# Performance work log

Hardware: AMD Instinct MI355X
Metric: run time of the kernel (lower is better)

The kernel has to match this reference:

```python
import jax, jax.numpy as jnp
import numpy as np

B, C_IN, T, IMG, P = 4, 3, 8, 224, 16
E, DEPTH, D_INNER, N_ST, DT_R, K = 384, 24, 768, 16, 24, 4
HP = IMG // P
NP_ = HP * HP          # 196 patches per frame
L = T * NP_            # 1568 tokens
EPS = 1e-5


def setup_inputs():
    key = jax.random.key(0)
    ks = jax.random.split(key, 24)
    r = lambda k, s, sc=0.02: jax.random.normal(k, s, jnp.float32) * sc
    inp = {
        "x": jax.random.normal(ks[0], (B, C_IN, T, IMG, IMG), jnp.float32),
        "patch_w": r(ks[1], (E, C_IN, 1, P, P)),
        "patch_b": jnp.zeros((E,), jnp.float32),
        "pos_embed": r(ks[2], (NP_, E)),
        "temporal_pos": r(ks[3], (T, E)),
        "imp_w1": r(ks[4], (E, E)),
        "imp_b1": jnp.zeros((E,), jnp.float32),
        "imp_w2": r(ks[5], (1, E)),
        "imp_b2": jnp.zeros((1,), jnp.float32),
        "in_w": r(ks[6], (DEPTH, 2 * D_INNER, E)),
        "out_w": r(ks[7], (DEPTH, E, D_INNER)),
        "norm_w": jnp.ones((DEPTH, E), jnp.float32),
        "norm_f_w": jnp.ones((E,), jnp.float32),
    }
    A_row = jnp.log(jnp.arange(1, N_ST + 1, dtype=jnp.float32))  # S4D-real init
    for i, sfx in enumerate(["", "_b"]):
        b = 8 + 4 * i
        inp["conv_w" + sfx] = r(ks[b], (DEPTH, D_INNER, K), 0.1)
        inp["conv_b" + sfx] = jnp.zeros((DEPTH, D_INNER), jnp.float32)
        inp["xp_w" + sfx] = r(ks[b + 1], (DEPTH, DT_R + 2 * N_ST, D_INNER))
        inp["dt_w" + sfx] = r(ks[b + 2], (DEPTH, D_INNER, DT_R), 0.01)
        inp["dt_b" + sfx] = jax.random.uniform(ks[b + 3], (DEPTH, D_INNER), jnp.float32, -4.6, -2.3)
        inp["A_log" + sfx] = jnp.tile(A_row, (DEPTH, D_INNER, 1))
        inp["D" + sfx] = jnp.ones((DEPTH, D_INNER), jnp.float32)
    return inp


def rmsnorm(x, w):
    x = x.astype(jnp.float32)
    return x * jax.lax.rsqrt(jnp.mean(x * x, axis=-1, keepdims=True) + EPS) * w


def causal_conv1d(x, w, b):
    # x: [B,L,D]; depthwise causal conv with kernel K
    xt = x.transpose(0, 2, 1)  # B D L
    y = jax.lax.conv_general_dilated(
        xt, w[:, None, :], (1,), [(K - 1, 0)],
        dimension_numbers=("NCH", "OIH", "NCH"), feature_group_count=D_INNER)
    return (y + b[None, :, None]).transpose(0, 2, 1)


def selective_scan(xt, dt, Bm, Cm, A, Dp):
    # xt,dt: [B,L,D]; Bm,Cm: [B,L,N]; A: [D,N]
    def step(h, ins):
        dt_t, x_t, B_t, C_t = ins  # [B,D],[B,D],[B,N],[B,N]
        h = h * jnp.exp(dt_t[..., None] * A) + (dt_t * x_t)[..., None] * B_t[:, None, :]
        return h, jnp.einsum('bdn,bn->bd', h, C_t)
    h0 = jnp.zeros((xt.shape[0], D_INNER, N_ST), xt.dtype)
    xs = (dt.transpose(1, 0, 2), xt.transpose(1, 0, 2),
          Bm.transpose(1, 0, 2), Cm.transpose(1, 0, 2))
    _, ys = jax.lax.scan(step, h0, xs)
    return ys.transpose(1, 0, 2) + xt * Dp


def mamba_dir(xc, z, cw, cb, xpw, dtw, dtb, Alog, Dp):
    xt = jax.nn.silu(causal_conv1d(xc, cw, cb))
    dbc = jnp.einsum('bld,ed->ble', xt, xpw)
    dt_low = dbc[..., :DT_R]
    Bm = dbc[..., DT_R:DT_R + N_ST]
    Cm = dbc[..., DT_R + N_ST:]
    dt = jax.nn.softplus(jnp.einsum('blr,dr->bld', dt_low, dtw) + dtb)
    y = selective_scan(xt, dt, Bm, Cm, -jnp.exp(Alog), Dp)
    return y * jax.nn.silu(z)


def mamba_block(h, p):
    xz = jnp.einsum('ble,fe->blf', h, p['in_w'])
    xc, z = xz[..., :D_INNER], xz[..., D_INNER:]
    yf = mamba_dir(xc, z, p['conv_w'], p['conv_b'], p['xp_w'], p['dt_w'], p['dt_b'], p['A_log'], p['D'])
    flip = lambda t: t[:, ::-1, :]
    yb = flip(mamba_dir(flip(xc), flip(z), p['conv_w_b'], p['conv_b_b'], p['xp_w_b'],
                        p['dt_w_b'], p['dt_b_b'], p['A_log_b'], p['D_b']))
    return jnp.einsum('bld,ed->ble', yf + yb, p['out_w'])


def _encoder(x, patch_w, patch_b, pos_embed, temporal_pos, imp_w1, imp_b1, imp_w2, imp_b2,
             in_w, out_w, norm_w, norm_f_w,
             conv_w, conv_b, xp_w, dt_w, dt_b, A_log, D,
             conv_w_b, conv_b_b, xp_w_b, dt_w_b, dt_b_b, A_log_b, D_b, mixer=mamba_block):
    Bn = x.shape[0]
    # PatchEmbed: Conv3d kernel (1,P,P) stride (1,P,P) == patchify + matmul
    xp = x.reshape(Bn, C_IN, T, HP, P, HP, P)
    xp = xp.transpose(0, 2, 3, 5, 1, 4, 6).reshape(Bn, T, NP_, C_IN * P * P)
    tok = xp @ patch_w.reshape(E, C_IN * P * P).T + patch_b  # [B,T,N,E]
    tok = tok + pos_embed[None, None] + temporal_pos[None, :, None, :]
    xseq = tok.reshape(Bn, L, E)
    # token importance gating
    h1 = jax.nn.relu(xseq @ imp_w1.T + imp_b1)
    logits = (h1 @ imp_w2.T + imp_b2)[..., 0]  # [B,L]
    xseq = xseq * jax.nn.sigmoid(logits)[..., None]
    stacked = {'in_w': in_w, 'out_w': out_w, 'norm_w': norm_w,
               'conv_w': conv_w, 'conv_b': conv_b, 'xp_w': xp_w, 'dt_w': dt_w,
               'dt_b': dt_b, 'A_log': A_log, 'D': D,
               'conv_w_b': conv_w_b, 'conv_b_b': conv_b_b, 'xp_w_b': xp_w_b,
               'dt_w_b': dt_w_b, 'dt_b_b': dt_b_b, 'A_log_b': A_log_b, 'D_b': D_b}

    def layer_fn(carry, p):
        hidden, residual = carry
        residual = (hidden + residual).astype(jnp.float32)  # fused add-norm, prenorm
        hn = rmsnorm(residual, p['norm_w'])
        hidden = mixer(hn, p)
        return (hidden, residual), None

    (hidden, residual), _ = jax.lax.scan(layer_fn, (xseq, jnp.zeros_like(xseq)), stacked)
    feats = rmsnorm(hidden + residual, norm_f_w)
    return feats, logits


def reference(x, patch_w, patch_b, pos_embed, temporal_pos, imp_w1, imp_b1, imp_w2, imp_b2,
              in_w, out_w, norm_w, norm_f_w,
              conv_w, conv_b, xp_w, dt_w, dt_b, A_log, D,
              conv_w_b, conv_b_b, xp_w_b, dt_w_b, dt_b_b, A_log_b, D_b):
    return _encoder(x, patch_w, patch_b, pos_embed, temporal_pos, imp_w1, imp_b1, imp_w2, imp_b2,
                    in_w, out_w, norm_w, norm_f_w,
                    conv_w, conv_b, xp_w, dt_w, dt_b, A_log, D,
                    conv_w_b, conv_b_b, xp_w_b, dt_w_b, dt_b_b, A_log_b, D_b)
```

## Files before the change

### kernel.cpp

```cpp
#include <hip/hip_runtime.h>
#include <hip/hip_bf16.h>

#define LL 1568
#define EE 384
#define DD 768
#define BB 4

typedef float f32x4 __attribute__((ext_vector_type(4)));
typedef float f32x2 __attribute__((ext_vector_type(2)));
typedef unsigned short u16x2 __attribute__((ext_vector_type(2)));
typedef unsigned short u16x4 __attribute__((ext_vector_type(4)));
typedef unsigned short u16x8 __attribute__((ext_vector_type(8)));
typedef __bf16 bf16x8 __attribute__((ext_vector_type(8)));

__device__ inline unsigned short f2bf(float f) {
    unsigned int u = __builtin_bit_cast(unsigned int, f);
    u += 0x7fffu + ((u >> 16) & 1u);
    return (unsigned short)(u >> 16);
}
__device__ inline float bf2f(unsigned short u) {
    unsigned int v = ((unsigned int)u) << 16;
    return __builtin_bit_cast(float, v);
}
__device__ inline float silu_f(float v) { return v / (1.f + __expf(-v)); }
__device__ inline float exp2_f(float v) { return __builtin_amdgcn_exp2f(v); }

__global__ __launch_bounds__(256) void k_cvt(const float* __restrict__ src,
                                             unsigned short* __restrict__ dst, int n4) {
    int i = blockIdx.x * 256 + threadIdx.x;
    int stride = gridDim.x * 256;
    for (; i < n4; i += stride) {
        f32x4 v = *(const f32x4*)(src + (size_t)i * 4);
        u16x4 o;
#pragma unroll
        for (int j = 0; j < 4; j++) o[j] = f2bf(v[j]);
        *(u16x4*)(dst + (size_t)i * 4) = o;
    }
}

__global__ __launch_bounds__(256) void k_pad_xpw(const float* __restrict__ src,
                                                 unsigned short* __restrict__ dst) {
    const int total = 24 * 64 * 768;
    for (int i = blockIdx.x * 256 + threadIdx.x; i < total; i += gridDim.x * 256) {
        int l = i / (64 * 768);
        int r = (i / 768) % 64;
        int dcol = i % 768;
        dst[i] = (r < 56) ? f2bf(src[((size_t)l * 56 + r) * 768 + dcol]) : (unsigned short)0;
    }
}

__global__ __launch_bounds__(256) void k_pad_dtw(const float* __restrict__ src,
                                                 unsigned short* __restrict__ dst) {
    const int total = 24 * 768 * 32;
    for (int i = blockIdx.x * 256 + threadIdx.x; i < total; i += gridDim.x * 256) {
        int kk = i & 31;
        int nrow = i >> 5;
        dst[i] = (kk < 24) ? f2bf(src[(size_t)nrow * 24 + kk]) : (unsigned short)0;
    }
}

__global__ __launch_bounds__(256) void k_patch(const float* __restrict__ x,
                                               unsigned short* __restrict__ patches) {
    int bid = blockIdx.x;
    int b = bid / LL, rr = bid % LL, t = rr / 196, pp = rr % 196, hp = pp / 14, wp = pp % 14;
    for (int k = threadIdx.x; k < 768; k += 256) {
        int c = k >> 8, rem = k & 255, i = rem >> 4, j = rem & 15;
        patches[(size_t)bid * 768 + k] =
            f2bf(x[(((size_t)(b * 3 + c) * 8 + t) * 224 + hp * 16 + i) * 224 + wp * 16 + j]);
    }
}

template <int EPI, bool ASUM, bool OUTBF>
__global__ __launch_bounds__(256) void k_gemm(
    const unsigned short* __restrict__ A, const unsigned short* __restrict__ A2,
    const unsigned short* __restrict__ W, const unsigned short* __restrict__ W2,
    float* __restrict__ C, unsigned short* __restrict__ Cb, int K, int ldc,
    const float* __restrict__ bias, const float* __restrict__ bias2,
    const float* __restrict__ pos, const float* __restrict__ tpos) {
    const int tid = threadIdx.x;
    const int m0 = blockIdx.y * 128;
    const int n0 = blockIdx.x * 128;
    __shared__ unsigned short As[128 * 40];
    __shared__ unsigned short Ws[128 * 40];
    const int sr = tid >> 2;
    const int skc = tid & 3;

    const unsigned short* Wp = W;
    const float* biasp = bias;
    if constexpr (EPI == 3) {
        if (m0 >= 6272) { Wp = W2; biasp = bias2; }
    }

    f32x4 acc[4][4];
#pragma unroll
    for (int mi = 0; mi < 4; mi++)
#pragma unroll
        for (int ni = 0; ni < 4; ni++) acc[mi][ni] = (f32x4){0.f, 0.f, 0.f, 0.f};

    const int lane = tid & 63;
    const int wv = tid >> 6;
    const int wm = (wv & 1) << 6;
    const int wn = (wv >> 1) << 6;
    const int lr = lane & 15;
    const int kg = lane >> 4;

    u16x8 ar[2], wr_[2];
    auto loadT = [&](int kt) {
#pragma unroll
        for (int i = 0; i < 2; i++) {
            size_t ka = (size_t)(m0 + sr + 64 * i) * K + kt * 32 + skc * 8;
            u16x8 v = *(const u16x8*)(A + ka);
            if constexpr (ASUM) {
                u16x8 v2 = *(const u16x8*)(A2 + ka);
#pragma unroll
                for (int j = 0; j < 8; j++) v[j] = f2bf(bf2f(v[j]) + bf2f(v2[j]));
            }
            ar[i] = v;
            wr_[i] = *(const u16x8*)(Wp + (size_t)(n0 + sr + 64 * i) * K + kt * 32 + skc * 8);
        }
    };

    const int nK = K >> 5;
    loadT(0);
    for (int kt = 0; kt < nK; ++kt) {
#pragma unroll
        for (int i = 0; i < 2; i++) {
            *(u16x8*)&As[(sr + 64 * i) * 40 + skc * 8] = ar[i];
            *(u16x8*)&Ws[(sr + 64 * i) * 40 + skc * 8] = wr_[i];
        }
        __syncthreads();
        if (kt + 1 < nK) loadT(kt + 1);
        bf16x8 af[4], bfm[4];
#pragma unroll
        for (int mi = 0; mi < 4; mi++)
            af[mi] = *(const bf16x8*)&As[(wm + mi * 16 + lr) * 40 + kg * 8];
#pragma unroll
        for (int ni = 0; ni < 4; ni++)
            bfm[ni] = *(const bf16x8*)&Ws[(wn + ni * 16 + lr) * 40 + kg * 8];
#pragma unroll
        for (int mi = 0; mi < 4; mi++)
#pragma unroll
            for (int ni = 0; ni < 4; ni++)
                acc[mi][ni] = __builtin_amdgcn_mfma_f32_16x16x32_bf16(af[mi], bfm[ni], acc[mi][ni], 0, 0, 0);
        __syncthreads();
    }

#pragma unroll
    for (int mi = 0; mi < 4; mi++)
#pragma unroll
        for (int ni = 0; ni < 4; ni++)
#pragma unroll
            for (int j = 0; j < 4; j++) {
                int m = m0 + wm + mi * 16 + kg * 4 + j;
                int n = n0 + wn + ni * 16 + lr;
                float v = acc[mi][ni][j];
                if constexpr (EPI == 1) {
                    int rr = m % LL;
                    int t = rr / 196, p = rr % 196;
                    v += bias[n] + pos[p * EE + n] + tpos[t * EE + n];
                    C[(size_t)m * ldc + n] = v;
                    Cb[(size_t)m * ldc + n] = f2bf(v);
                } else if constexpr (EPI == 2) {
                    v += bias[n];
                    v = fmaxf(v, 0.f);
                    C[(size_t)m * ldc + n] = v;
                } else if constexpr (EPI == 3) {
                    v += biasp[n];
                    float sp = (v > 20.f) ? v : log1pf(__expf(v));
                    Cb[(size_t)m * ldc + n] = f2bf(sp);
                } else {
                    if constexpr (OUTBF)
                        Cb[(size_t)m * ldc + n] = f2bf(v);
                    else
                        C[(size_t)m * ldc + n] = v;
                }
            }
}

__global__ __launch_bounds__(64) void k_logits(const float* __restrict__ h1, const float* __restrict__ w2,
                                               const float* __restrict__ b2, float* __restrict__ xseq,
                                               float* __restrict__ logits_out) {
    int row = blockIdx.x;
    int lane = threadIdx.x;
    float acc = 0.f;
#pragma unroll
    for (int i = 0; i < 6; i++) {
        int e = lane + i * 64;
        acc += h1[(size_t)row * EE + e] * w2[e];
    }
#pragma unroll
    for (int off = 32; off >= 1; off >>= 1) acc += __shfl_xor(acc, off);
    float logit = acc + b2[0];
    if (lane == 0) logits_out[row] = logit;
    float sg = 1.f / (1.f + __expf(-logit));
#pragma unroll
    for (int i = 0; i < 6; i++) {
        int e = lane + i * 64;
        xseq[(size_t)row * EE + e] *= sg;
    }
}

template <bool OBF>
__global__ __launch_bounds__(256) void k_norm(const float* __restrict__ hidden, float* __restrict__ resid,
                                              const float* __restrict__ wn, float* __restrict__ outf,
                                              unsigned short* __restrict__ outb,
                                              int first, int writeResid) {
    int row = blockIdx.x * 4 + (threadIdx.x >> 6);
    int lane = threadIdx.x & 63;
    size_t base = (size_t)row * EE;
    float v[6];
    float ss = 0.f;
#pragma unroll
    for (int i = 0; i < 6; i++) {
        int e = lane + i * 64;
        float h = hidden[base + e];
        float r = first ? 0.f : resid[base + e];
        float s = h + r;
        v[i] = s;
        ss += s * s;
    }
#pragma unroll
    for (int off = 32; off >= 1; off >>= 1) ss += __shfl_xor(ss, off);
    if (writeResid) {
#pragma unroll
        for (int i = 0; i < 6; i++) resid[base + lane + i * 64] = v[i];
    }
    float sc = rsqrtf(ss * (1.f / 384.f) + 1e-5f);
#pragma unroll
    for (int i = 0; i < 6; i++) {
        int e = lane + i * 64;
        float o = v[i] * sc * wn[e];
        if constexpr (OBF)
            outb[base + e] = f2bf(o);
        else
            outf[base + e] = o;
    }
}

__global__ __launch_bounds__(256) void k_conv(
    const unsigned short* __restrict__ xz,
    const float* __restrict__ cw_f, const float* __restrict__ cb_f,
    const float* __restrict__ cw_b, const float* __restrict__ cb_b,
    unsigned short* __restrict__ xtb) {
    const int tid = threadIdx.x;
    if (tid >= 192) return;
    const int b = blockIdx.y, dir = blockIdx.z;
    const float* cw = dir ? cw_b : cw_f;
    const float* cb = dir ? cb_b : cb_f;
    const int o = tid % 96, tg = tid / 96;
    const int t0 = blockIdx.x * 16 + tg * 8;
    const int d0 = o * 8;
    const size_t xzb = (size_t)b * LL * 1536;
    const size_t obase = ((size_t)dir * BB + b) * LL;

    f32x4 wq[8];
    float bv[8];
#pragma unroll
    for (int j = 0; j < 8; j++) {
        wq[j] = *(const f32x4*)&cw[(d0 + j) * 4];
        bv[j] = cb[d0 + j];
    }

    auto loadrow = [&](int t) -> u16x8 {
        if (t < 0) return (u16x8){0, 0, 0, 0, 0, 0, 0, 0};
        int phys = dir ? (LL - 1 - t) : t;
        return *(const u16x8*)&xz[xzb + (size_t)phys * 1536 + d0];
    };

    float f0[8], f1[8], f2[8];
    u16x8 v;
    v = loadrow(t0 - 3);
#pragma unroll
    for (int j = 0; j < 8; j++) f0[j] = bf2f(v[j]);
    v = loadrow(t0 - 2);
#pragma unroll
    for (int j = 0; j < 8; j++) f1[j] = bf2f(v[j]);
    v = loadrow(t0 - 1);
#pragma unroll
    for (int j = 0; j < 8; j++) f2[j] = bf2f(v[j]);

    for (int s = 0; s < 8; ++s) {
        int t = t0 + s;
        v = loadrow(t);
        float f3[8];
        u16x8 outv;
#pragma unroll
        for (int j = 0; j < 8; j++) {
            f3[j] = bf2f(v[j]);
            float cv = wq[j][0] * f0[j] + wq[j][1] * f1[j] + wq[j][2] * f2[j] + wq[j][3] * f3[j] + bv[j];
            outv[j] = f2bf(silu_f(cv));
        }
        *(u16x8*)&xtb[(obase + t) * 768 + d0] = outv;
#pragma unroll
        for (int j = 0; j < 8; j++) { f0[j] = f1[j]; f1[j] = f2[j]; f2[j] = f3[j]; }
    }
}

__global__ __launch_bounds__(256) void k_dbc(
    const unsigned short* __restrict__ xtb,
    const unsigned short* __restrict__ xpwb_f, const unsigned short* __restrict__ xpwb_b,
    unsigned short* __restrict__ dtlow, float* __restrict__ Bm, float* __restrict__ Cm) {
    const int tid = threadIdx.x;
    const int m0 = blockIdx.x * 64;
    const unsigned short* W = (m0 >= 6272) ? xpwb_b : xpwb_f;
    __shared__ unsigned short As[64 * 40];
    __shared__ unsigned short Ws[64 * 40];
    const int sr = tid >> 2, skc = tid & 3;
    const int lane = tid & 63, wv = tid >> 6;
    const int lr = lane & 15, kg = lane >> 4;

    f32x4 acc[4];
#pragma unroll
    for (int mi = 0; mi < 4; mi++) acc[mi] = (f32x4){0.f, 0.f, 0.f, 0.f};

    u16x8 ar, wr_;
    auto loadT = [&](int kt) {
        ar = *(const u16x8*)(xtb + (size_t)(m0 + sr) * 768 + kt * 32 + skc * 8);
        wr_ = *(const u16x8*)(W + (size_t)sr * 768 + kt * 32 + skc * 8);
    };
    loadT(0);
    for (int kt = 0; kt < 24; ++kt) {
        *(u16x8*)&As[sr * 40 + skc * 8] = ar;
        *(u16x8*)&Ws[sr * 40 + skc * 8] = wr_;
        __syncthreads();
        if (kt + 1 < 24) loadT(kt + 1);
        bf16x8 bfm = *(const bf16x8*)&Ws[(wv * 16 + lr) * 40 + kg * 8];
#pragma unroll
        for (int mi = 0; mi < 4; mi++) {
            bf16x8 af = *(const bf16x8*)&As[(mi * 16 + lr) * 40 + kg * 8];
            acc[mi] = __builtin_amdgcn_mfma_f32_16x16x32_bf16(af, bfm, acc[mi], 0, 0, 0);
        }
        __syncthreads();
    }
#pragma unroll
    for (int mi = 0; mi < 4; mi++)
#pragma unroll
        for (int j = 0; j < 4; j++) {
            int row = m0 + mi * 16 + kg * 4 + j;
            int cc = wv * 16 + lr;
            float vv = acc[mi][j];
            if (cc < 24) dtlow[(size_t)row * 32 + cc] = f2bf(vv);
            else if (cc < 40) Bm[(size_t)row * 16 + (cc - 24)] = vv;
            else if (cc < 56) Cm[(size_t)row * 16 + (cc - 40)] = vv;
            else dtlow[(size_t)row * 32 + (cc - 32)] = 0;
        }
}

__global__ __launch_bounds__(1024) void k_scan(
    const unsigned short* __restrict__ xtb, const unsigned short* __restrict__ dtb,
    const unsigned short* __restrict__ xz,
    const float* __restrict__ Bmat, const float* __restrict__ Cmat,
    const float* __restrict__ Alog_f, const float* __restrict__ Alog_b,
    const float* __restrict__ Dp_f, const float* __restrict__ Dp_b,
    unsigned short* __restrict__ ybuf) {
    const int tid = threadIdx.x;
    const int dl = tid & 31, c = tid >> 5;
    const int d = blockIdx.x * 32 + dl;
    const int b = blockIdx.y, dir = blockIdx.z;
    const float* Alog = dir ? Alog_b : Alog_f;
    const float* Dp = dir ? Dp_b : Dp_f;
    const int t0 = c * 49;

    __shared__ float Ssh[32][32][17];
    __shared__ float sdt_sh[32][32];

    float an[16];
#pragma unroll
    for (int n = 0; n < 16; n++) an[n] = -__expf(Alog[d * 16 + n]) * 1.44269504f;
    bool unif = (an[0] != 0.f);
#pragma unroll
    for (int n = 1; n < 16; n++) {
        float r = an[n] / an[0];
        unif = unif && (fabsf(r - (float)(n + 1)) < 1e-3f);
    }
    const float an0 = an[0];
    float Dd = Dp[d];

    const size_t dbase = ((size_t)dir * BB + b) * LL;
    const size_t rowb = dbase * 768 + d;

    f32x2 S2[8];
#pragma unroll
    for (int k = 0; k < 8; k++) S2[k] = (f32x2){0.f, 0.f};
    float sumdt = 0.f;

    for (int s = 0; s < 49; ++s) {
        int t = t0 + s;
        float xt = bf2f(xtb[rowb + (size_t)t * 768]);
        float dtv = bf2f(dtb[rowb + (size_t)t * 768]);
        sumdt += dtv;
        float dtx = dtv * xt;
        const f32x4* Bp = (const f32x4*)(Bmat + (dbase + t) * 16);
        f32x4 Bq[4] = {Bp[0], Bp[1], Bp[2], Bp[3]};
        const f32x2* B2 = (const f32x2*)Bq;
        f32x2 dtx2 = {dtx, dtx};
        if (unif) {
            float p = exp2_f(dtv * an0);
            float q = p * p;
            f32x2 q2 = {q, q};
            f32x2 pw2[8];
            pw2[0] = (f32x2){p, q};
#pragma unroll
            for (int j = 1; j < 8; j++) pw2[j] = pw2[j - 1] * q2;
#pragma unroll
            for (int k = 0; k < 8; k++) S2[k] = S2[k] * pw2[k] + dtx2 * B2[k];
        } else {
#pragma unroll
            for (int n = 0; n < 16; n++) {
                float e = exp2_f(dtv * an[n]);
                float sv = S2[n >> 1][n & 1];
                S2[n >> 1][n & 1] = sv * e + dtx * ((const float*)Bq)[n];
            }
        }
    }
#pragma unroll
    for (int n = 0; n < 16; n++) Ssh[c][dl][n] = S2[n >> 1][n & 1];
    sdt_sh[c][dl] = sumdt;
    __syncthreads();

    if (tid < 512) {
        int cdl = tid & 31, n2 = tid >> 5;
        float a_n = -__expf(Alog[(blockIdx.x * 32 + cdl) * 16 + n2]) * 1.44269504f;
        float H = 0.f;
#pragma unroll
        for (int c2 = 0; c2 < 32; c2++) {
            float P = exp2_f(a_n * sdt_sh[c2][cdl]);
            float tmp = Ssh[c2][cdl][n2];
            Ssh[c2][cdl][n2] = H;
            H = H * P + tmp;
        }
    }
    __syncthreads();

#pragma unroll
    for (int n = 0; n < 16; n++) S2[n >> 1][n & 1] = Ssh[c][dl][n];
    for (int s = 0; s < 49; ++s) {
        int t = t0 + s;
        float xt = bf2f(xtb[rowb + (size_t)t * 768]);
        float dtv = bf2f(dtb[rowb + (size_t)t * 768]);
        float dtx = dtv * xt;
        const f32x4* Bp = (const f32x4*)(Bmat + (dbase + t) * 16);
        f32x4 Bq[4] = {Bp[0], Bp[1], Bp[2], Bp[3]};
        const f32x4* Cp = (const f32x4*)(Cmat + (dbase + t) * 16);
        f32x4 Cq[4] = {Cp[0], Cp[1], Cp[2], Cp[3]};
        const f32x2* B2 = (const f32x2*)Bq;
        const f32x2* C2 = (const f32x2*)Cq;
        f32x2 dtx2 = {dtx, dtx};
        f32x2 y2 = {0.f, 0.f};
        if (unif) {
            float p = exp2_f(dtv * an0);
            float q = p * p;
            f32x2 q2 = {q, q};
            f32x2 pw2[8];
            pw2[0] = (f32x2){p, q};
#pragma unroll
            for (int j = 1; j < 8; j++) pw2[j] = pw2[j - 1] * q2;
#pragma unroll
            for (int k = 0; k < 8; k++) {
                S2[k] = S2[k] * pw2[k] + dtx2 * B2[k];
                y2 = y2 + S2[k] * C2[k];
            }
        } else {
#pragma unroll
            for (int n = 0; n < 16; n++) {
                float e = exp2_f(dtv * an[n]);
                float sv = S2[n >> 1][n & 1];
                sv = sv * e + dtx * ((const float*)Bq)[n];
                S2[n >> 1][n & 1] = sv;
                y2[n & 1] += sv * ((const float*)Cq)[n];
            }
        }
        float y = y2[0] + y2[1] + xt * Dd;
        int pt = dir ? (LL - 1 - t) : t;
        float zv = bf2f(xz[((size_t)b * LL + pt) * 1536 + 768 + d]);
        ybuf[rowb + (size_t)pt * 768] = f2bf(y * silu_f(zv));
    }
}

extern "C" void kernel_launch(void* const* d_in, const int* in_sizes, int n_in,
                              void* d_out, int out_size, void* d_ws, size_t ws_size,
                              hipStream_t stream) {
    const float* x        = (const float*)d_in[0];
    const float* patch_w  = (const float*)d_in[1];
    const float* patch_b  = (const float*)d_in[2];
    const float* pos_emb  = (const float*)d_in[3];
    const float* tpos     = (const float*)d_in[4];
    const float* imp_w1   = (const float*)d_in[5];
    const float* imp_b1   = (const float*)d_in[6];
    const float* imp_w2   = (const float*)d_in[7];
    const float* imp_b2   = (const float*)d_in[8];
    const float* in_w     = (const float*)d_in[9];
    const float* out_w    = (const float*)d_in[10];
    const float* norm_w   = (const float*)d_in[11];
    const float* norm_f_w = (const float*)d_in[12];
    const float* conv_w   = (const float*)d_in[13];
    const float* conv_b   = (const float*)d_in[14];
    const float* xp_w     = (const float*)d_in[15];
    const float* dt_w     = (const float*)d_in[16];
    const float* dt_b     = (const float*)d_in[17];
    const float* A_log    = (const float*)d_in[18];
    const float* Dp       = (const float*)d_in[19];
    const float* conv_w_b = (const float*)d_in[20];
    const float* conv_b_b = (const float*)d_in[21];
    const float* xp_w_b   = (const float*)d_in[22];
    const float* dt_w_b   = (const float*)d_in[23];
    const float* dt_b_b   = (const float*)d_in[24];
    const float* A_log_b  = (const float*)d_in[25];
    const float* D_b      = (const float*)d_in[26];

    float* out = (float*)d_out;
    float* logits_out = out + 2408448;

    char* wsb = (char*)d_ws;
    size_t off = 0;
    auto carve = [&](size_t bytes) { char* p = wsb + off; off += bytes; return p; };

    unsigned short* in_wb    = (unsigned short*)carve(28311552);
    unsigned short* out_wb   = (unsigned short*)carve(14155776);
    unsigned short* patch_wb = (unsigned short*)carve(589824);
    unsigned short* imp_w1b  = (unsigned short*)carve(294912);
    unsigned short* xpwb_f   = (unsigned short*)carve(2359296);
    unsigned short* xpwb_b   = (unsigned short*)carve(2359296);
    unsigned short* dtwb_f   = (unsigned short*)carve(1179648);
    unsigned short* dtwb_b   = (unsigned short*)carve(1179648);
    float*          hidden   = (float*)carve(9633792);
    float*          resid    = (float*)carve(9633792);
    unsigned short* hn       = (unsigned short*)carve(4816896);
    unsigned short* xzb      = (unsigned short*)carve(19267584);
    unsigned short* xtb      = (unsigned short*)carve(19267584);
    unsigned short* g_dt     = (unsigned short*)carve(19267584);
    unsigned short* dtlow    = (unsigned short*)carve(802816);
    float*          Bm       = (float*)carve(802816);
    float*          Cm       = (float*)carve(802816);
    unsigned short* ybuf     = (unsigned short*)carve(19267584);

    float*          h1       = (float*)xtb;
    unsigned short* hidb     = (unsigned short*)g_dt;
    unsigned short* patches  = (unsigned short*)ybuf;

    k_cvt<<<2048, 256, 0, stream>>>(in_w, in_wb, 3538944);
    k_cvt<<<2048, 256, 0, stream>>>(out_w, out_wb, 1769472);
    k_cvt<<<288, 256, 0, stream>>>(patch_w, patch_wb, 73728);
    k_cvt<<<144, 256, 0, stream>>>(imp_w1, imp_w1b, 36864);
    k_pad_xpw<<<1024, 256, 0, stream>>>(xp_w, xpwb_f);
    k_pad_xpw<<<1024, 256, 0, stream>>>(xp_w_b, xpwb_b);
    k_pad_dtw<<<1024, 256, 0, stream>>>(dt_w, dtwb_f);
    k_pad_dtw<<<1024, 256, 0, stream>>>(dt_w_b, dtwb_b);

    k_patch<<<6272, 256, 0, stream>>>(x, patches);
    k_gemm<1, false, false><<<dim3(3, 49), 256, 0, stream>>>(patches, nullptr, patch_wb, nullptr,
                                                             hidden, hidb, 768, 384,
                                                             patch_b, nullptr, pos_emb, tpos);
    k_gemm<2, false, false><<<dim3(3, 49), 256, 0, stream>>>(hidb, nullptr, imp_w1b, nullptr,
                                                             h1, nullptr, 384, 384,
                                                             imp_b1, nullptr, nullptr, nullptr);
    k_logits<<<6272, 64, 0, stream>>>(h1, imp_w2, imp_b2, hidden, logits_out);

    for (int l = 0; l < 24; ++l) {
        k_norm<true><<<1568, 256, 0, stream>>>(hidden, resid, norm_w + l * 384, nullptr, hn,
                                               (l == 0) ? 1 : 0, 1);
        k_gemm<0, false, true><<<dim3(12, 49), 256, 0, stream>>>(hn, nullptr, in_wb + (size_t)l * 589824,
                                                                 nullptr, nullptr, xzb, 384, 1536,
                                                                 nullptr, nullptr, nullptr, nullptr);
        k_conv<<<dim3(98, 4, 2), 256, 0, stream>>>(xzb, conv_w + l * 3072, conv_b + l * 768,
                                                   conv_w_b + l * 3072, conv_b_b + l * 768, xtb);
        k_dbc<<<196, 256, 0, stream>>>(xtb, xpwb_f + (size_t)l * 49152, xpwb_b + (size_t)l * 49152,
                                       dtlow, Bm, Cm);
        k_gemm<3, false, true><<<dim3(6, 98), 256, 0, stream>>>(dtlow, nullptr,
                                                                dtwb_f + (size_t)l * 24576,
                                                                dtwb_b + (size_t)l * 24576,
                                                                nullptr, g_dt, 32, 768,
                                                                dt_b + l * 768, dt_b_b + l * 768,
                                                                nullptr, nullptr);
        k_scan<<<dim3(24, 4, 2), 1024, 0, stream>>>(
            xtb, g_dt, xzb, Bm, Cm,
            A_log + l * 12288, A_log_b + l * 12288,
            Dp + l * 768, D_b + l * 768,
            ybuf);
        k_gemm<0, true, false><<<dim3(3, 49), 256, 0, stream>>>(ybuf, ybuf + 4816896,
                                                                out_wb + (size_t)l * 294912, nullptr,
                                                                hidden, nullptr, 768, 384,
                                                                nullptr, nullptr, nullptr, nullptr);
    }
    k_norm<false><<<1568, 256, 0, stream>>>(hidden, resid, norm_f_w, out, nullptr, 0, 0);
}
```

Before: 5.129 ms.

## Fuse dt projection into x_proj kernel and process two channels per scan thread

The dt low-rank projection plus softplus GEMM is folded into k_dbc. The 64x32 dt_low tile is staged in shared memory and multiplied against the dt weights with MFMA inside the same block, which drops a kernel launch and the dtlow round trip through global memory. Separately, k_scan now uses 512 threads with each thread handling two adjacent channels, giving 32-bit vectorized loads and stores and more independent work per thread. The cost is fewer resident threads for the scan and a serialized 12-tile dt loop per block in k_dbc, which has only 196 blocks.

```diff
diff --git a/kernel.cpp b/kernel.cpp
--- a/kernel.cpp
+++ b/kernel.cpp
@@ -73,9 +73,9 @@
 template <int EPI, bool ASUM, bool OUTBF>
 __global__ __launch_bounds__(256) void k_gemm(
     const unsigned short* __restrict__ A, const unsigned short* __restrict__ A2,
-    const unsigned short* __restrict__ W, const unsigned short* __restrict__ W2,
+    const unsigned short* __restrict__ W,
     float* __restrict__ C, unsigned short* __restrict__ Cb, int K, int ldc,
-    const float* __restrict__ bias, const float* __restrict__ bias2,
+    const float* __restrict__ bias,
     const float* __restrict__ pos, const float* __restrict__ tpos) {
     const int tid = threadIdx.x;
     const int m0 = blockIdx.y * 128;
@@ -85,12 +85,6 @@
     const int sr = tid >> 2;
     const int skc = tid & 3;
 
-    const unsigned short* Wp = W;
-    const float* biasp = bias;
-    if constexpr (EPI == 3) {
-        if (m0 >= 6272) { Wp = W2; biasp = bias2; }
-    }
-
     f32x4 acc[4][4];
 #pragma unroll
     for (int mi = 0; mi < 4; mi++)
@@ -116,7 +110,7 @@
                 for (int j = 0; j < 8; j++) v[j] = f2bf(bf2f(v[j]) + bf2f(v2[j]));
             }
             ar[i] = v;
-            wr_[i] = *(const u16x8*)(Wp + (size_t)(n0 + sr + 64 * i) * K + kt * 32 + skc * 8);
+            wr_[i] = *(const u16x8*)(W + (size_t)(n0 + sr + 64 * i) * K + kt * 32 + skc * 8);
         }
     };
 
@@ -164,10 +158,6 @@
                     v += bias[n];
                     v = fmaxf(v, 0.f);
                     C[(size_t)m * ldc + n] = v;
-                } else if constexpr (EPI == 3) {
-                    v += biasp[n];
-                    float sp = (v > 20.f) ? v : log1pf(__expf(v));
-                    Cb[(size_t)m * ldc + n] = f2bf(sp);
                 } else {
                     if constexpr (OUTBF)
                         Cb[(size_t)m * ldc + n] = f2bf(v);
@@ -299,12 +289,16 @@
 __global__ __launch_bounds__(256) void k_dbc(
     const unsigned short* __restrict__ xtb,
     const unsigned short* __restrict__ xpwb_f, const unsigned short* __restrict__ xpwb_b,
-    unsigned short* __restrict__ dtlow, float* __restrict__ Bm, float* __restrict__ Cm) {
+    const unsigned short* __restrict__ dtwb_f, const unsigned short* __restrict__ dtwb_b,
+    const float* __restrict__ dtb_f, const float* __restrict__ dtb_b,
+    unsigned short* __restrict__ g_dt, float* __restrict__ Bm, float* __restrict__ Cm) {
     const int tid = threadIdx.x;
     const int m0 = blockIdx.x * 64;
-    const unsigned short* W = (m0 >= 6272) ? xpwb_b : xpwb_f;
+    const bool bwd = (m0 >= 6272);
+    const unsigned short* W = bwd ? xpwb_b : xpwb_f;
     __shared__ unsigned short As[64 * 40];
     __shared__ unsigned short Ws[64 * 40];
+    __shared__ unsigned short Ds[64 * 40];
     const int sr = tid >> 2, skc = tid & 3;
     const int lane = tid & 63, wv = tid >> 6;
     const int lr = lane & 15, kg = lane >> 4;
@@ -336,17 +330,54 @@
     for (int mi = 0; mi < 4; mi++)
 #pragma unroll
         for (int j = 0; j < 4; j++) {
-            int row = m0 + mi * 16 + kg * 4 + j;
+            int r = mi * 16 + kg * 4 + j;
+            int row = m0 + r;
             int cc = wv * 16 + lr;
             float vv = acc[mi][j];
-            if (cc < 24) dtlow[(size_t)row * 32 + cc] = f2bf(vv);
-            else if (cc < 40) Bm[(size_t)row * 16 + (cc - 24)] = vv;
-            else if (cc < 56) Cm[(size_t)row * 16 + (cc - 40)] = vv;
-            else dtlow[(size_t)row * 32 + (cc - 32)] = 0;
-        }
-}
-
-__global__ __launch_bounds__(1024) void k_scan(
+            if (cc < 32) Ds[r * 40 + cc] = (cc < 24) ? f2bf(vv) : (unsigned short)0;
+            if (cc >= 24 && cc < 40) Bm[(size_t)row * 16 + (cc - 24)] = vv;
+            else if (cc >= 40 && cc < 56) Cm[(size_t)row * 16 + (cc - 40)] = vv;
+        }
+    __syncthreads();
+
+    const unsigned short* dtw = bwd ? dtwb_b : dtwb_f;
+    const float* dbias = bwd ? dtb_b : dtb_f;
+    bf16x8 af2[4];
+#pragma unroll
+    for (int mi = 0; mi < 4; mi++)
+        af2[mi] = *(const bf16x8*)&Ds[(mi * 16 + lr) * 40 + kg * 8];
+    for (int nt = wv; nt < 12; nt += 4) {
+        int n0 = nt * 64;
+        f32x4 acc2[4][4];
+#pragma unroll
+        for (int mi = 0; mi < 4; mi++)
+#pragma unroll
+            for (int ni = 0; ni < 4; ni++) acc2[mi][ni] = (f32x4){0.f, 0.f, 0.f, 0.f};
+        bf16x8 bfr[4];
+#pragma unroll
+        for (int ni = 0; ni < 4; ni++)
+            bfr[ni] = *(const bf16x8*)(dtw + (size_t)(n0 + ni * 16 + lr) * 32 + kg * 8);
+#pragma unroll
+        for (int mi = 0; mi < 4; mi++)
+#pragma unroll
+            for (int ni = 0; ni < 4; ni++)
+                acc2[mi][ni] = __builtin_amdgcn_mfma_f32_16x16x32_bf16(af2[mi], bfr[ni], acc2[mi][ni], 0, 0, 0);
+#pragma unroll
+        for (int mi = 0; mi < 4; mi++)
+#pragma unroll
+            for (int ni = 0; ni < 4; ni++)
+#pragma unroll
+                for (int j = 0; j < 4; j++) {
+                    int r = mi * 16 + kg * 4 + j;
+                    int n = n0 + ni * 16 + lr;
+                    float v = acc2[mi][ni][j] + dbias[n];
+                    float sp = (v > 20.f) ? v : log1pf(__expf(v));
+                    g_dt[(size_t)(m0 + r) * 768 + n] = f2bf(sp);
+                }
+    }
+}
+
+__global__ __launch_bounds__(512) void k_scan(
     const unsigned short* __restrict__ xtb, const unsigned short* __restrict__ dtb,
     const unsigned short* __restrict__ xz,
     const float* __restrict__ Bmat, const float* __restrict__ Cmat,
@@ -354,8 +385,8 @@
     const float* __restrict__ Dp_f, const float* __restrict__ Dp_b,
     unsigned short* __restrict__ ybuf) {
     const int tid = threadIdx.x;
-    const int dl = tid & 31, c = tid >> 5;
-    const int d = blockIdx.x * 32 + dl;
+    const int dl = tid & 15, c = tid >> 4;
+    const int d0 = blockIdx.x * 32 + dl * 2;
     const int b = blockIdx.y, dir = blockIdx.z;
     const float* Alog = dir ? Alog_b : Alog_f;
     const float* Dp = dir ? Dp_b : Dp_f;
@@ -364,61 +395,77 @@
     __shared__ float Ssh[32][32][17];
     __shared__ float sdt_sh[32][32];
 
-    float an[16];
-#pragma unroll
-    for (int n = 0; n < 16; n++) an[n] = -__expf(Alog[d * 16 + n]) * 1.44269504f;
-    bool unif = (an[0] != 0.f);
+    float anA[16], anB[16];
+#pragma unroll
+    for (int n = 0; n < 16; n++) {
+        anA[n] = -__expf(Alog[d0 * 16 + n]) * 1.44269504f;
+        anB[n] = -__expf(Alog[(d0 + 1) * 16 + n]) * 1.44269504f;
+    }
+    bool unif = (anA[0] != 0.f) && (anB[0] != 0.f);
 #pragma unroll
     for (int n = 1; n < 16; n++) {
-        float r = an[n] / an[0];
-        unif = unif && (fabsf(r - (float)(n + 1)) < 1e-3f);
-    }
-    const float an0 = an[0];
-    float Dd = Dp[d];
+        float rA = anA[n] / anA[0];
+        float rB = anB[n] / anB[0];
+        unif = unif && (fabsf(rA - (float)(n + 1)) < 1e-3f) && (fabsf(rB - (float)(n + 1)) < 1e-3f);
+    }
+    const float a0A = anA[0], a0B = anB[0];
+    float DdA = Dp[d0], DdB = Dp[d0 + 1];
 
     const size_t dbase = ((size_t)dir * BB + b) * LL;
-    const size_t rowb = dbase * 768 + d;
-
-    f32x2 S2[8];
-#pragma unroll
-    for (int k = 0; k < 8; k++) S2[k] = (f32x2){0.f, 0.f};
-    float sumdt = 0.f;
+    const size_t rowb = dbase * 768 + d0;
+
+    f32x2 SA[8], SB[8];
+#pragma unroll
+    for (int k = 0; k < 8; k++) { SA[k] = (f32x2){0.f, 0.f}; SB[k] = (f32x2){0.f, 0.f}; }
+    float sumA = 0.f, sumB = 0.f;
 
     for (int s = 0; s < 49; ++s) {
         int t = t0 + s;
-        float xt = bf2f(xtb[rowb + (size_t)t * 768]);
-        float dtv = bf2f(dtb[rowb + (size_t)t * 768]);
-        sumdt += dtv;
-        float dtx = dtv * xt;
+        unsigned int xv = *(const unsigned int*)&xtb[rowb + (size_t)t * 768];
+        unsigned int dv = *(const unsigned int*)&dtb[rowb + (size_t)t * 768];
+        float xtA = bf2f((unsigned short)xv), xtB = bf2f((unsigned short)(xv >> 16));
+        float dtA = bf2f((unsigned short)dv), dtB = bf2f((unsigned short)(dv >> 16));
+        sumA += dtA; sumB += dtB;
+        float dxA = dtA * xtA, dxB = dtB * xtB;
         const f32x4* Bp = (const f32x4*)(Bmat + (dbase + t) * 16);
         f32x4 Bq[4] = {Bp[0], Bp[1], Bp[2], Bp[3]};
         const f32x2* B2 = (const f32x2*)Bq;
-        f32x2 dtx2 = {dtx, dtx};
+        f32x2 dxA2 = {dxA, dxA}, dxB2 = {dxB, dxB};
         if (unif) {
-            float p = exp2_f(dtv * an0);
-            float q = p * p;
-            f32x2 q2 = {q, q};
-            f32x2 pw2[8];
-            pw2[0] = (f32x2){p, q};
-#pragma unroll
-            for (int j = 1; j < 8; j++) pw2[j] = pw2[j - 1] * q2;
-#pragma unroll
-            for (int k = 0; k < 8; k++) S2[k] = S2[k] * pw2[k] + dtx2 * B2[k];
+            float pA = exp2_f(dtA * a0A), pB = exp2_f(dtB * a0B);
+            float qA = pA * pA, qB = pB * pB;
+            f32x2 qA2 = {qA, qA}, qB2 = {qB, qB};
+            f32x2 pwA[8], pwB[8];
+            pwA[0] = (f32x2){pA, qA};
+            pwB[0] = (f32x2){pB, qB};
+#pragma unroll
+            for (int j = 1; j < 8; j++) { pwA[j] = pwA[j - 1] * qA2; pwB[j] = pwB[j - 1] * qB2; }
+#pragma unroll
+            for (int k = 0; k < 8; k++) {
+                SA[k] = SA[k] * pwA[k] + dxA2 * B2[k];
+                SB[k] = SB[k] * pwB[k] + dxB2 * B2[k];
+            }
         } else {
 #pragma unroll
             for (int n = 0; n < 16; n++) {
-                float e = exp2_f(dtv * an[n]);
-                float sv = S2[n >> 1][n & 1];
-                S2[n >> 1][n & 1] = sv * e + dtx * ((const float*)Bq)[n];
+                float bqv = ((const float*)Bq)[n];
+                float eA = exp2_f(dtA * anA[n]);
+                float eB = exp2_f(dtB * anB[n]);
+                SA[n >> 1][n & 1] = SA[n >> 1][n & 1] * eA + dxA * bqv;
+                SB[n >> 1][n & 1] = SB[n >> 1][n & 1] * eB + dxB * bqv;
             }
         }
     }
 #pragma unroll
-    for (int n = 0; n < 16; n++) Ssh[c][dl][n] = S2[n >> 1][n & 1];
-    sdt_sh[c][dl] = sumdt;
+    for (int n = 0; n < 16; n++) {
+        Ssh[c][dl * 2][n] = SA[n >> 1][n & 1];
+        Ssh[c][dl * 2 + 1][n] = SB[n >> 1][n & 1];
+    }
+    sdt_sh[c][dl * 2] = sumA;
+    sdt_sh[c][dl * 2 + 1] = sumB;
     __syncthreads();
 
-    if (tid < 512) {
+    {
         int cdl = tid & 31, n2 = tid >> 5;
         float a_n = -__expf(Alog[(blockIdx.x * 32 + cdl) * 16 + n2]) * 1.44269504f;
         float H = 0.f;
@@ -433,47 +480,64 @@
     __syncthreads();
 
 #pragma unroll
-    for (int n = 0; n < 16; n++) S2[n >> 1][n & 1] = Ssh[c][dl][n];
+    for (int n = 0; n < 16; n++) {
+        SA[n >> 1][n & 1] = Ssh[c][dl * 2][n];
+        SB[n >> 1][n & 1] = Ssh[c][dl * 2 + 1][n];
+    }
     for (int s = 0; s < 49; ++s) {
         int t = t0 + s;
-        float xt = bf2f(xtb[rowb + (size_t)t * 768]);
-        float dtv = bf2f(dtb[rowb + (size_t)t * 768]);
-        float dtx = dtv * xt;
+        unsigned int xv = *(const unsigned int*)&xtb[rowb + (size_t)t * 768];
+        unsigned int dv = *(const unsigned int*)&dtb[rowb + (size_t)t * 768];
+        float xtA = bf2f((unsigned short)xv), xtB = bf2f((unsigned short)(xv >> 16));
+        float dtA = bf2f((unsigned short)dv), dtB = bf2f((unsigned short)(dv >> 16));
+        float dxA = dtA * xtA, dxB = dtB * xtB;
         const f32x4* Bp = (const f32x4*)(Bmat + (dbase + t) * 16);
         f32x4 Bq[4] = {Bp[0], Bp[1], Bp[2], Bp[3]};
         const f32x4* Cp = (const f32x4*)(Cmat + (dbase + t) * 16);
         f32x4 Cq[4] = {Cp[0], Cp[1], Cp[2], Cp[3]};
         const f32x2* B2 = (const f32x2*)Bq;
         const f32x2* C2 = (const f32x2*)Cq;
-        f32x2 dtx2 = {dtx, dtx};
-        f32x2 y2 = {0.f, 0.f};
+        f32x2 dxA2 = {dxA, dxA}, dxB2 = {dxB, dxB};
+        f32x2 yA2 = {0.f, 0.f}, yB2 = {0.f, 0.f};
         if (unif) {
-            float p = exp2_f(dtv * an0);
-            float q = p * p;
-            f32x2 q2 = {q, q};
-            f32x2 pw2[8];
-            pw2[0] = (f32x2){p, q};
-#pragma unroll
-            for (int j = 1; j < 8; j++) pw2[j] = pw2[j - 1] * q2;
+            float pA = exp2_f(dtA * a0A), pB = exp2_f(dtB * a0B);
+            float qA = pA * pA, qB = pB * pB;
+            f32x2 qA2 = {qA, qA}, qB2 = {qB, qB};
+            f32x2 pwA[8], pwB[8];
+            pwA[0] = (f32x2){pA, qA};
+            pwB[0] = (f32x2){pB, qB};
+#pragma unroll
+            for (int j = 1; j < 8; j++) { pwA[j] = pwA[j - 1] * qA2; pwB[j] = pwB[j - 1] * qB2; }
 #pragma unroll
             for (int k = 0; k < 8; k++) {
-                S2[k] = S2[k] * pw2[k] + dtx2 * B2[k];
-                y2 = y2 + S2[k] * C2[k];
+                SA[k] = SA[k] * pwA[k] + dxA2 * B2[k];
+                SB[k] = SB[k] * pwB[k] + dxB2 * B2[k];
+                yA2 = yA2 + SA[k] * C2[k];
+                yB2 = yB2 + SB[k] * C2[k];
             }
         } else {
 #pragma unroll
             for (int n = 0; n < 16; n++) {
-                float e = exp2_f(dtv * an[n]);
-                float sv = S2[n >> 1][n & 1];
-                sv = sv * e + dtx * ((const float*)Bq)[n];
-                S2[n >> 1][n & 1] = sv;
-                y2[n & 1] += sv * ((const float*)Cq)[n];
+                float bqv = ((const float*)Bq)[n];
+                float cqv = ((const float*)Cq)[n];
+                float eA = exp2_f(dtA * anA[n]);
+                float eB = exp2_f(dtB * anB[n]);
+                float sA = SA[n >> 1][n & 1] * eA + dxA * bqv;
+                float sB = SB[n >> 1][n & 1] * eB + dxB * bqv;
+                SA[n >> 1][n & 1] = sA;
+                SB[n >> 1][n & 1] = sB;
+                yA2[n & 1] += sA * cqv;
+                yB2[n & 1] += sB * cqv;
             }
         }
-        float y = y2[0] + y2[1] + xt * Dd;
+        float yA = yA2[0] + yA2[1] + xtA * DdA;
+        float yB = yB2[0] + yB2[1] + xtB * DdB;
         int pt = dir ? (LL - 1 - t) : t;
-        float zv = bf2f(xz[((size_t)b * LL + pt) * 1536 + 768 + d]);
-        ybuf[rowb + (size_t)pt * 768] = f2bf(y * silu_f(zv));
+        unsigned int zv2 = *(const unsigned int*)&xz[((size_t)b * LL + pt) * 1536 + 768 + d0];
+        float zA = bf2f((unsigned short)zv2), zB = bf2f((unsigned short)(zv2 >> 16));
+        unsigned int yo = (unsigned int)f2bf(yA * silu_f(zA)) |
+                          ((unsigned int)f2bf(yB * silu_f(zB)) << 16);
+        *(unsigned int*)&ybuf[rowb + (size_t)pt * 768] = yo;
     }
 }
 
@@ -529,7 +593,6 @@
     unsigned short* xzb      = (unsigned short*)carve(19267584);
     unsigned short* xtb      = (unsigned short*)carve(19267584);
     unsigned short* g_dt     = (unsigned short*)carve(19267584);
-    unsigned short* dtlow    = (unsigned short*)carve(802816);
     float*          Bm       = (float*)carve(802816);
     float*          Cm       = (float*)carve(802816);
     unsigned short* ybuf     = (unsigned short*)carve(19267584);
@@ -548,39 +611,36 @@
     k_pad_dtw<<<1024, 256, 0, stream>>>(dt_w_b, dtwb_b);
 
     k_patch<<<6272, 256, 0, stream>>>(x, patches);
-    k_gemm<1, false, false><<<dim3(3, 49), 256, 0, stream>>>(patches, nullptr, patch_wb, nullptr,
+    k_gemm<1, false, false><<<dim3(3, 49), 256, 0, stream>>>(patches, nullptr, patch_wb,
                                                              hidden, hidb, 768, 384,
-                                                             patch_b, nullptr, pos_emb, tpos);
-    k_gemm<2, false, false><<<dim3(3, 49), 256, 0, stream>>>(hidb, nullptr, imp_w1b, nullptr,
+                                                             patch_b, pos_emb, tpos);
+    k_gemm<2, false, false><<<dim3(3, 49), 256, 0, stream>>>(hidb, nullptr, imp_w1b,
                                                              h1, nullptr, 384, 384,
-                                                             imp_b1, nullptr, nullptr, nullptr);
+                                                             imp_b1, nullptr, nullptr);
     k_logits<<<6272, 64, 0, stream>>>(h1, imp_w2, imp_b2, hidden, logits_out);
 
     for (int l = 0; l < 24; ++l) {
         k_norm<true><<<1568, 256, 0, stream>>>(hidden, resid, norm_w + l * 384, nullptr, hn,
                                                (l == 0) ? 1 : 0, 1);
-        k_gemm<0, false, true><<<dim3(12, 49), 256, 0, stream>>>(hn, nullptr, in_wb + (size_t)l * 589824,
-                                                                 nullptr, nullptr, xzb, 384, 1536,
-                                                                 nullptr, nullptr, nullptr, nullptr);
+        k_gemm<0, false, true><<<dim3(12, 49), 256, 0, stream>>>(hn, nullptr,
+                                                                 in_wb + (size_t)l * 589824,
+                                                                 nullptr, xzb, 384, 1536,
+                                                                 nullptr, nullptr, nullptr);
         k_conv<<<dim3(98, 4, 2), 256, 0, stream>>>(xzb, conv_w + l * 3072, conv_b + l * 768,
                                                    conv_w_b + l * 3072, conv_b_b + l * 768, xtb);
         k_dbc<<<196, 256, 0, stream>>>(xtb, xpwb_f + (size_t)l * 49152, xpwb_b + (size_t)l * 49152,
-                                       dtlow, Bm, Cm);
-        k_gemm<3, false, true><<<dim3(6, 98), 256, 0, stream>>>(dtlow, nullptr,
-                                                                dtwb_f + (size_t)l * 24576,
-                                                                dtwb_b + (size_t)l * 24576,
-                                                                nullptr, g_dt, 32, 768,
-                                                                dt_b + l * 768, dt_b_b + l * 768,
-                                                                nullptr, nullptr);
-        k_scan<<<dim3(24, 4, 2), 1024, 0, stream>>>(
+                                       dtwb_f + (size_t)l * 24576, dtwb_b + (size_t)l * 24576,
+                                       dt_b + l * 768, dt_b_b + l * 768,
+                                       g_dt, Bm, Cm);
+        k_scan<<<dim3(24, 4, 2), 512, 0, stream>>>(
             xtb, g_dt, xzb, Bm, Cm,
             A_log + l * 12288, A_log_b + l * 12288,
             Dp + l * 768, D_b + l * 768,
             ybuf);
         k_gemm<0, true, false><<<dim3(3, 49), 256, 0, stream>>>(ybuf, ybuf + 4816896,
-                                                                out_wb + (size_t)l * 294912, nullptr,
+                                                                out_wb + (size_t)l * 294912,
                                                                 hidden, nullptr, 768, 384,
-                                                                nullptr, nullptr, nullptr, nullptr);
+                                                                nullptr, nullptr, nullptr);
     }
     k_norm<false><<<1568, 256, 0, stream>>>(hidden, resid, norm_f_w, out, nullptr, 0, 0);
 }
```

After: 5.280 ms. 1.03x slower.
